# Optimization experiments

Hardware: AMD Instinct MI355X
Metric: run time of the kernel (lower is better)

## Reference

```python
import jax, jax.numpy as jnp
import numpy as np

B, N, A = 32, 1024, 256          # batch, n_entities, n_agents
D_IN, D_H, H = 256, 256, 8       # input_dim, hidden_dim, n_heads
SCALE = 1.0 / np.sqrt(D_H)
EPS = 1e-12


def setup_inputs() -> dict:
    key = jax.random.key(0)
    ks = jax.random.split(key, 7)
    x = jax.random.normal(ks[0], (B, N, D_IN), dtype=jnp.float32)
    # binary visibility mask [batch, n_agents, n_entities]
    m = (jax.random.uniform(ks[1], (B, A, N)) > 0.5).astype(jnp.float32)
    # encoder Linear(input_dim, hidden_dim): weight [out,in], bias [out]
    W_enc = jax.random.normal(ks[2], (D_H, D_IN), dtype=jnp.float32) / np.sqrt(D_IN)
    b_enc = jnp.zeros((D_H,), dtype=jnp.float32)
    # per-head projection matrices stacked [H, D_H, D_H] (torch.randn init)
    WQ = jax.random.normal(ks[3], (H, D_H, D_H), dtype=jnp.float32)
    WK = jax.random.normal(ks[4], (H, D_H, D_H), dtype=jnp.float32)
    WV = jax.random.normal(ks[5], (H, D_H, D_H), dtype=jnp.float32)
    return {"x": x, "m": m, "W_enc": W_enc, "b_enc": b_enc, "WQ": WQ, "WK": WK, "WV": WV}


def reference(x, m, W_enc, b_enc, WQ, WK, WV):
    # encode: LeakyReLU then Linear
    h = jnp.einsum('bni,oi->bno', jax.nn.leaky_relu(x), W_enc) + b_enc  # [B,N,D_H]
    n_agents = m.shape[1]
    ha = h[:, :n_agents]                                   # [B,A,D_H]
    # per-head projections, heads vectorized
    Q = jnp.einsum('bad,hde->bhae', ha, WQ)                # [B,H,A,D_H]
    K = jnp.einsum('bnd,hde->bhne', h, WK)                 # [B,H,N,D_H]
    V = jnp.einsum('bnd,hde->bhne', h, WV)                 # [B,H,N,D_H]
    S = jnp.einsum('bhae,bhne->bhan', Q, K) * SCALE        # [B,H,A,N]
    P = jax.nn.softmax(S, axis=-1)
    P = P * m[:, None]                                     # post-softmax mask
    prob = P / (jnp.sum(P, axis=-1, keepdims=True) + EPS)  # renormalize
    z = jnp.einsum('bhan,bhne->bhae', prob, V)             # [B,H,A,D_H]
    return jnp.mean(z, axis=1)                             # [B,A,D_H]
```

## Files before the change

kernel.cpp:

```cpp
#include <hip/hip_runtime.h>
#include <math.h>

namespace {
constexpr int B_N  = 32;
constexpr int SEQ  = 1024;
constexpr int AG   = 256;
constexpr int D    = 256;
constexpr int NH   = 8;
constexpr float SCALE = 0.0625f;
constexpr float EPS   = 1e-12f;

constexpr size_t HHI_OFF  = 0;
constexpr size_t HLO_OFF  = 16777216;
constexpr size_t HT_OFF   = 33554432;
constexpr size_t MTHI_OFF = 50331648;
constexpr size_t MTLO_OFF = 51380224;
constexpr size_t MB_OFF   = 52428800;
constexpr size_t WVT_OFF  = 53477376;
constexpr size_t Z16_OFF  = 54525952;
}

typedef __attribute__((ext_vector_type(8))) short short8;
typedef __attribute__((ext_vector_type(4))) float floatx4;
#define MFMA_BF(A,B,C) __builtin_amdgcn_mfma_f32_16x16x32_bf16(A,B,C,0,0,0)

__device__ __forceinline__ unsigned short bf16_rtne(float f) {
    unsigned u = __float_as_uint(f);
    u += 0x7fffu + ((u >> 16) & 1u);
    return (unsigned short)(u >> 16);
}
__device__ __forceinline__ float bf16_tof(unsigned short h) {
    return __uint_as_float(((unsigned)h) << 16);
}
__device__ __forceinline__ void async16(void* lds, const void* g) {
    __builtin_amdgcn_global_load_lds(
        (const __attribute__((address_space(1))) unsigned int*)g,
        (__attribute__((address_space(3))) unsigned int*)lds,
        16, 0, 0);
}

__global__ __launch_bounds__(256) void enc_kernel(
    const float* __restrict__ x, const float* __restrict__ W_enc,
    const float* __restrict__ b_enc,
    ushort* __restrict__ h_hi, ushort* __restrict__ h_lo)
{
    __shared__ float AsT[32][68];
    __shared__ float BsT[32][68];
    const int t  = threadIdx.x;
    const int tx = t & 15, ty = t >> 4;
    const int col0 = blockIdx.x * 64;
    const int row0 = blockIdx.y * 64;

    float acc[4][4];
#pragma unroll
    for (int r = 0; r < 4; ++r)
#pragma unroll
        for (int c = 0; c < 4; ++c) acc[r][c] = 0.f;

    for (int k0 = 0; k0 < 256; k0 += 32) {
        __syncthreads();
#pragma unroll
        for (int ss = 0; ss < 2; ++ss) {
            int flat = t + 256 * ss;
            int rr = flat >> 3, k4 = flat & 7;
            float4 v = *(const float4*)(x + (size_t)(row0 + rr) * 256 + k0 + k4 * 4);
            v.x = v.x > 0.f ? v.x : 0.01f * v.x;
            v.y = v.y > 0.f ? v.y : 0.01f * v.y;
            v.z = v.z > 0.f ? v.z : 0.01f * v.z;
            v.w = v.w > 0.f ? v.w : 0.01f * v.w;
            AsT[k4*4+0][rr] = v.x; AsT[k4*4+1][rr] = v.y;
            AsT[k4*4+2][rr] = v.z; AsT[k4*4+3][rr] = v.w;
            float4 wv = *(const float4*)(W_enc + (size_t)(col0 + rr) * 256 + k0 + k4 * 4);
            BsT[k4*4+0][rr] = wv.x; BsT[k4*4+1][rr] = wv.y;
            BsT[k4*4+2][rr] = wv.z; BsT[k4*4+3][rr] = wv.w;
        }
        __syncthreads();
#pragma unroll 8
        for (int kk = 0; kk < 32; ++kk) {
            float4 a4 = *(const float4*)&AsT[kk][ty * 4];
            float4 b4 = *(const float4*)&BsT[kk][tx * 4];
            const float ar[4] = {a4.x, a4.y, a4.z, a4.w};
            const float bc[4] = {b4.x, b4.y, b4.z, b4.w};
#pragma unroll
            for (int r = 0; r < 4; ++r)
#pragma unroll
                for (int c = 0; c < 4; ++c)
                    acc[r][c] = fmaf(ar[r], bc[c], acc[r][c]);
        }
    }

    float4 bv = *(const float4*)(b_enc + col0 + tx * 4);
    const float bb4[4] = {bv.x, bv.y, bv.z, bv.w};
#pragma unroll
    for (int r = 0; r < 4; ++r) {
        const int row = row0 + ty * 4 + r;
        ushort hi4[4], lo4[4];
#pragma unroll
        for (int c = 0; c < 4; ++c) {
            float v = acc[r][c] + bb4[c];
            hi4[c] = bf16_rtne(v);
            lo4[c] = bf16_rtne(v - bf16_tof(hi4[c]));
        }
        *(ushort4*)(h_hi + (size_t)row * 256 + col0 + tx * 4) =
            make_ushort4(hi4[0], hi4[1], hi4[2], hi4[3]);
        *(ushort4*)(h_lo + (size_t)row * 256 + col0 + tx * 4) =
            make_ushort4(lo4[0], lo4[1], lo4[2], lo4[3]);
    }
}

__global__ __launch_bounds__(256) void htrans_kernel(
    const ushort* __restrict__ h_hi, ushort* __restrict__ hT)
{
    __shared__ ushort T[64][72];
    const int t = threadIdx.x;
    const int n0 = blockIdx.x * 64, d0 = blockIdx.y * 64, b = blockIdx.z;
    {
        const int r = t >> 2, c = (t & 3) * 16;
        const ushort* src = h_hi + ((size_t)(b * 1024 + n0 + r)) * 256 + d0 + c;
        *(short8*)&T[r][c]     = *(const short8*)src;
        *(short8*)&T[r][c + 8] = *(const short8*)(src + 8);
    }
    __syncthreads();
    {
        const int dd = t >> 2, seg = (t & 3) * 16;
        ushort tmp[16];
#pragma unroll
        for (int j = 0; j < 16; ++j) tmp[j] = T[seg + j][dd];
        ushort* dst = hT + ((size_t)(b * 256 + d0 + dd)) * 1024 + n0 + seg;
        *(short8*)dst       = *(short8*)&tmp[0];
        *(short8*)(dst + 8) = *(short8*)&tmp[8];
    }
}

__global__ __launch_bounds__(256) void wvt_kernel(
    const float* __restrict__ WV, ushort* __restrict__ WVt)
{
    __shared__ float T[64][68];
    const int t = threadIdx.x;
    const int d0 = blockIdx.x * 64, e0 = blockIdx.y * 64, h = blockIdx.z;
    {
        const int r = t >> 2, c = (t & 3) * 16;
        const float* src = WV + ((size_t)(h * 256 + d0 + r)) * 256 + e0 + c;
#pragma unroll
        for (int j = 0; j < 4; ++j)
            *(float4*)&T[r][c + j * 4] = *(const float4*)(src + j * 4);
    }
    __syncthreads();
    {
        const int ee = t >> 2, seg = (t & 3) * 16;
        ushort tmp[16];
#pragma unroll
        for (int j = 0; j < 16; ++j) tmp[j] = bf16_rtne(T[seg + j][ee]);
        ushort* dst = WVt + ((size_t)(h * 256 + e0 + ee)) * 256 + d0 + seg;
        *(short8*)dst       = *(short8*)&tmp[0];
        *(short8*)(dst + 8) = *(short8*)&tmp[8];
    }
}

__global__ __launch_bounds__(256) void mprep_kernel(
    const float* __restrict__ WQ, const float* __restrict__ WK,
    ushort* __restrict__ Mt_hi, ushort* __restrict__ Mt_lo)
{
    __shared__ float AsT[32][68];
    __shared__ float BsT[32][68];
    const int t  = threadIdx.x;
    const int tx = t & 15, ty = t >> 4;
    const int col0 = blockIdx.x * 64;
    const int row0 = blockIdx.y * 64;
    const float* A  = WK + (size_t)blockIdx.z * 256 * 256;
    const float* Bm = WQ + (size_t)blockIdx.z * 256 * 256;
    ushort* Chi = Mt_hi + (size_t)blockIdx.z * 256 * 256;
    ushort* Clo = Mt_lo + (size_t)blockIdx.z * 256 * 256;

    float acc[4][4];
#pragma unroll
    for (int r = 0; r < 4; ++r)
#pragma unroll
        for (int c = 0; c < 4; ++c) acc[r][c] = 0.f;

    for (int k0 = 0; k0 < 256; k0 += 32) {
        __syncthreads();
#pragma unroll
        for (int ss = 0; ss < 2; ++ss) {
            int flat = t + 256 * ss;
            int rr = flat >> 3, k4 = flat & 7;
            float4 v = *(const float4*)(A + (size_t)(row0 + rr) * 256 + k0 + k4 * 4);
            AsT[k4*4+0][rr] = v.x; AsT[k4*4+1][rr] = v.y;
            AsT[k4*4+2][rr] = v.z; AsT[k4*4+3][rr] = v.w;
            float4 wv = *(const float4*)(Bm + (size_t)(col0 + rr) * 256 + k0 + k4 * 4);
            BsT[k4*4+0][rr] = wv.x; BsT[k4*4+1][rr] = wv.y;
            BsT[k4*4+2][rr] = wv.z; BsT[k4*4+3][rr] = wv.w;
        }
        __syncthreads();
#pragma unroll 8
        for (int kk = 0; kk < 32; ++kk) {
            float4 a4 = *(const float4*)&AsT[kk][ty * 4];
            float4 b4 = *(const float4*)&BsT[kk][tx * 4];
            const float ar[4] = {a4.x, a4.y, a4.z, a4.w};
            const float bc[4] = {b4.x, b4.y, b4.z, b4.w};
#pragma unroll
            for (int r = 0; r < 4; ++r)
#pragma unroll
                for (int c = 0; c < 4; ++c)
                    acc[r][c] = fmaf(ar[r], bc[c], acc[r][c]);
        }
    }
#pragma unroll
    for (int r = 0; r < 4; ++r) {
        const int row = row0 + ty * 4 + r;
        ushort hi4[4], lo4[4];
#pragma unroll
        for (int c = 0; c < 4; ++c) {
            float v = acc[r][c];
            hi4[c] = bf16_rtne(v);
            lo4[c] = bf16_rtne(v - bf16_tof(hi4[c]));
        }
        *(ushort4*)(Chi + (size_t)row * 256 + col0 + tx * 4) =
            make_ushort4(hi4[0], hi4[1], hi4[2], hi4[3]);
        *(ushort4*)(Clo + (size_t)row * 256 + col0 + tx * 4) =
            make_ushort4(lo4[0], lo4[1], lo4[2], lo4[3]);
    }
}

__global__ __launch_bounds__(256) void maskbits_kernel(
    const float* __restrict__ m, unsigned* __restrict__ mb)
{
    const int idx = blockIdx.x * 256 + threadIdx.x;
    const float4* src = (const float4*)(m + (size_t)idx * 32);
    unsigned wbits = 0;
#pragma unroll
    for (int i = 0; i < 8; ++i) {
        float4 v = src[i];
        wbits |= (v.x > 0.5f ? 1u : 0u) << (i * 4 + 0);
        wbits |= (v.y > 0.5f ? 1u : 0u) << (i * 4 + 1);
        wbits |= (v.z > 0.5f ? 1u : 0u) << (i * 4 + 2);
        wbits |= (v.w > 0.5f ? 1u : 0u) << (i * 4 + 3);
    }
    mb[idx] = wbits;
}

__global__ __launch_bounds__(256, 2) void attn_mfma(
    const ushort* __restrict__ h_hi, const ushort* __restrict__ h_lo,
    const ushort* __restrict__ hT,   const ushort* __restrict__ Mt_hi,
    const ushort* __restrict__ Mt_lo, const unsigned* __restrict__ mbits,
    ushort* __restrict__ zout)
{
    __shared__ __align__(16) char lds[54272];
    ushort* hS_hi = (ushort*)lds;
    ushort* hS_lo = (ushort*)(lds + 16384);
    ushort* hTS   = (ushort*)(lds + 32768);
    ushort* pP    = (ushort*)(lds + 49152);

    const int t    = threadIdx.x;
    const int wv   = t >> 6;
    const int lane = t & 63;
    const int l15  = lane & 15;
    const int quad = lane >> 4;
    const int f    = blockIdx.x;
    const int b    = (f & 7) + 8 * (f >> 8);
    const int r5   = (f >> 3) & 31;
    const int hh   = r5 >> 2;
    const int a0   = (r5 & 3) * 64;
    const int aw   = a0 + wv * 16;

    const ushort* hbh = h_hi + (size_t)b * SEQ * D;
    const ushort* hbl = h_lo + (size_t)b * SEQ * D;
    const ushort* hTb = hT   + (size_t)b * D * SEQ;

    floatx4 qac[16];
#pragma unroll
    for (int i = 0; i < 16; ++i) qac[i] = (floatx4){0.f, 0.f, 0.f, 0.f};

    for (int kc = 0; kc < 4; ++kc) {
        short8 Ah[2], Al[2];
#pragma unroll
        for (int kt = 0; kt < 2; ++kt) {
            const size_t ao = ((size_t)b * SEQ + aw + l15) * D +
                              kc * 64 + kt * 32 + quad * 8;
            Ah[kt] = *(const short8*)(h_hi + ao);
            Al[kt] = *(const short8*)(h_lo + ao);
        }
#pragma unroll
        for (int nt2 = 0; nt2 < 16; ++nt2) {
#pragma unroll
            for (int kt = 0; kt < 2; ++kt) {
                const size_t mo = ((size_t)hh * D + nt2 * 16 + l15) * D +
                                  kc * 64 + kt * 32 + quad * 8;
                short8 Bh = *(const short8*)(Mt_hi + mo);
                short8 Bl = *(const short8*)(Mt_lo + mo);
                qac[nt2] = MFMA_BF(Ah[kt], Bh, qac[nt2]);
                qac[nt2] = MFMA_BF(Al[kt], Bh, qac[nt2]);
                qac[nt2] = MFMA_BF(Ah[kt], Bl, qac[nt2]);
            }
        }
    }

    short8 Qhi[8], Qlo[8];
    {
        float* qscr = (float*)lds;
        for (int c = 0; c < 4; ++c) {
#pragma unroll
            for (int j = 0; j < 4; ++j)
#pragma unroll
                for (int r = 0; r < 4; ++r)
                    qscr[(wv * 16 + quad * 4 + r) * 68 + j * 16 + l15] = qac[c * 4 + j][r];
#pragma unroll
            for (int kt = 0; kt < 2; ++kt) {
                const float* pr = &qscr[(wv * 16 + l15) * 68 + kt * 32 + quad * 8];
                float ftmp[8];
                *(float4*)&ftmp[0] = *(const float4*)pr;
                *(float4*)&ftmp[4] = *(const float4*)(pr + 4);
                short8 hi, lo;
#pragma unroll
                for (int e = 0; e < 8; ++e) {
                    unsigned short hb = bf16_rtne(ftmp[e]);
                    hi[e] = (short)hb;
                    lo[e] = (short)bf16_rtne(ftmp[e] - bf16_tof(hb));
                }
                Qhi[c * 2 + kt] = hi;
                Qlo[c * 2 + kt] = lo;
            }
        }
    }

    floatx4 zac[16];
#pragma unroll
    for (int i = 0; i < 16; ++i) zac[i] = (floatx4){0.f, 0.f, 0.f, 0.f};
    float mx[4] = {-INFINITY, -INFINITY, -INFINITY, -INFINITY};
    float Za[4] = {0.f, 0.f, 0.f, 0.f};
    float Zm[4] = {0.f, 0.f, 0.f, 0.f};

    for (int nt = 0; nt < 32; ++nt) {
        const int n0 = nt * 32;
        __syncthreads();

#pragma unroll
        for (int i = 0; i < 4; ++i) {
            const int slot = wv * 256 + i * 64 + lane;
            const int row  = slot >> 5;
            const int p    = slot & 31;
            const int c    = p ^ (row & 7);
            const size_t go = (size_t)(n0 + row) * 256 + c * 8;
            const size_t lo_ = (size_t)(wv * 256 + i * 64) * 8;
            async16(hS_hi + lo_, hbh + go);
            async16(hS_lo + lo_, hbl + go);
        }
#pragma unroll
        for (int i = 0; i < 4; ++i) {
            const int slot = wv * 256 + i * 64 + lane;
            const int row  = slot >> 2;
            const int p    = slot & 3;
            const int c    = p ^ ((row >> 2) & 3);
            async16(hTS + (size_t)(wv * 256 + i * 64) * 8,
                    hTb + (size_t)row * 1024 + n0 + c * 8);
        }
        __syncthreads();

        floatx4 sac[2];
        sac[0] = (floatx4){0.f, 0.f, 0.f, 0.f};
        sac[1] = (floatx4){0.f, 0.f, 0.f, 0.f};
#pragma unroll
        for (int ks = 0; ks < 8; ++ks) {
            const int cg = ks * 4 + quad;
#pragma unroll
            for (int ntile = 0; ntile < 2; ++ntile) {
                const int row = ntile * 16 + l15;
                const int off = row * 256 + (cg ^ (row & 7)) * 8;
                short8 Bh = *(const short8*)&hS_hi[off];
                short8 Bl = *(const short8*)&hS_lo[off];
                sac[ntile] = MFMA_BF(Qhi[ks], Bh, sac[ntile]);
                sac[ntile] = MFMA_BF(Qlo[ks], Bh, sac[ntile]);
                sac[ntile] = MFMA_BF(Qhi[ks], Bl, sac[ntile]);
            }
        }

        float alr[4];
#pragma unroll
        for (int r = 0; r < 4; ++r) {
            const int a = a0 + wv * 16 + quad * 4 + r;
            const unsigned w0 = mbits[((size_t)b * AG + a) * (SEQ / 32) + nt];
            float l0 = sac[0][r] * SCALE, l1 = sac[1][r] * SCALE;
            float mt = fmaxf(l0, l1);
#pragma unroll
            for (int off = 1; off < 16; off <<= 1) mt = fmaxf(mt, __shfl_xor(mt, off));
            const float mxn = fmaxf(mx[r], mt);
            const float al  = __expf(mx[r] - mxn);
            float e0 = __expf(l0 - mxn), e1 = __expf(l1 - mxn);
            float p0 = ((w0 >> l15) & 1u)        ? e0 : 0.f;
            float p1 = ((w0 >> (16 + l15)) & 1u) ? e1 : 0.f;
            float za = e0 + e1;
            float zm = p0 + p1;
#pragma unroll
            for (int off = 1; off < 16; off <<= 1) {
                za += __shfl_xor(za, off);
                zm += __shfl_xor(zm, off);
            }
            Za[r] = Za[r] * al + za;
            Zm[r] = Zm[r] * al + zm;
            mx[r] = mxn;
            pP[(wv * 16 + quad * 4 + r) * 40 + l15]      = bf16_rtne(p0);
            pP[(wv * 16 + quad * 4 + r) * 40 + 16 + l15] = bf16_rtne(p1);
            alr[r] = al;
        }
#pragma unroll
        for (int dt = 0; dt < 16; ++dt) {
            zac[dt][0] *= alr[0]; zac[dt][1] *= alr[1];
            zac[dt][2] *= alr[2]; zac[dt][3] *= alr[3];
        }

        short8 Pf = *(const short8*)&pP[(wv * 16 + l15) * 40 + quad * 8];
#pragma unroll
        for (int dt = 0; dt < 16; ++dt) {
            const int row = dt * 16 + l15;
            const int p   = quad ^ ((row >> 2) & 3);
            short8 Bf = *(const short8*)&hTS[row * 32 + p * 8];
            zac[dt] = MFMA_BF(Pf, Bf, zac[dt]);
        }
    }

#pragma unroll
    for (int r = 0; r < 4; ++r) {
        const int a = a0 + wv * 16 + quad * 4 + r;
        const float inv = 1.0f / (Zm[r] + EPS * Za[r]);
        ushort* zr = zout + (((size_t)b * NH + hh) * AG + a) * D;
#pragma unroll
        for (int dt = 0; dt < 16; ++dt)
            zr[dt * 16 + l15] = bf16_rtne(zac[dt][r] * inv);
    }
}

__global__ __launch_bounds__(256) void out_mfma(
    const ushort* __restrict__ z16, const ushort* __restrict__ WVt,
    float* __restrict__ out)
{
    const int t    = threadIdx.x;
    const int wv   = t >> 6;
    const int lane = t & 63;
    const int l15  = lane & 15;
    const int quad = lane >> 4;
    const int e0 = blockIdx.x * 64;
    const int a0 = blockIdx.y * 64;
    const int b  = blockIdx.z;
    const int aw = a0 + wv * 16;

    floatx4 acc[4];
#pragma unroll
    for (int i = 0; i < 4; ++i) acc[i] = (floatx4){0.f, 0.f, 0.f, 0.f};

#pragma unroll 4
    for (int c = 0; c < 64; ++c) {
        const int hh = c >> 3, d0 = (c & 7) * 32;
        short8 Af = *(const short8*)(z16 +
            (((size_t)b * NH + hh) * AG + aw + l15) * D + d0 + quad * 8);
#pragma unroll
        for (int et = 0; et < 4; ++et) {
            short8 Bf = *(const short8*)(WVt +
                ((size_t)hh * D + e0 + et * 16 + l15) * D + d0 + quad * 8);
            acc[et] = MFMA_BF(Af, Bf, acc[et]);
        }
    }
#pragma unroll
    for (int et = 0; et < 4; ++et)
#pragma unroll
        for (int r = 0; r < 4; ++r)
            out[((size_t)b * AG + aw + quad * 4 + r) * D + e0 + et * 16 + l15] =
                acc[et][r] * 0.125f;
}

extern "C" void kernel_launch(void* const* d_in, const int* in_sizes, int n_in,
                              void* d_out, int out_size, void* d_ws, size_t ws_size,
                              hipStream_t stream)
{
    (void)in_sizes; (void)n_in; (void)out_size; (void)ws_size;
    const float* x     = (const float*)d_in[0];
    const float* m     = (const float*)d_in[1];
    const float* W_enc = (const float*)d_in[2];
    const float* b_enc = (const float*)d_in[3];
    const float* WQ    = (const float*)d_in[4];
    const float* WK    = (const float*)d_in[5];
    const float* WV    = (const float*)d_in[6];
    float* out = (float*)d_out;
    char* ws = (char*)d_ws;

    ushort*   h_hi  = (ushort*)(ws + HHI_OFF);
    ushort*   h_lo  = (ushort*)(ws + HLO_OFF);
    ushort*   hT    = (ushort*)(ws + HT_OFF);
    ushort*   Mt_hi = (ushort*)(ws + MTHI_OFF);
    ushort*   Mt_lo = (ushort*)(ws + MTLO_OFF);
    unsigned* mbits = (unsigned*)(ws + MB_OFF);
    ushort*   WVt   = (ushort*)(ws + WVT_OFF);
    ushort*   z16   = (ushort*)(ws + Z16_OFF);

    enc_kernel<<<dim3(4, 512, 1), dim3(256), 0, stream>>>(
        x, W_enc, b_enc, h_hi, h_lo);
    mprep_kernel<<<dim3(4, 4, NH), dim3(256), 0, stream>>>(WQ, WK, Mt_hi, Mt_lo);
    maskbits_kernel<<<dim3(1024, 1, 1), dim3(256), 0, stream>>>(m, mbits);
    htrans_kernel<<<dim3(16, 4, B_N), dim3(256), 0, stream>>>(h_hi, hT);
    wvt_kernel<<<dim3(4, 4, NH), dim3(256), 0, stream>>>(WV, WVt);
    attn_mfma<<<dim3(1024, 1, 1), dim3(256), 0, stream>>>(
        h_hi, h_lo, hT, Mt_hi, Mt_lo, mbits, z16);
    out_mfma<<<dim3(4, 4, B_N), dim3(256), 0, stream>>>(z16, WVt, out);
}
```

Before: 607.3 us.

## Fuse prep kernels into one launch and share K/V tiles across two heads

Four small preprocessing kernels (mask bit-packing, h transpose, WV transpose, WQ/WK product) are merged into one launch that dispatches on block index. This removes launch gaps between them. The attention kernel now uses 512-thread blocks, so two heads share each block and each staged h/hT tile in LDS. That halves global-to-LDS traffic per head and halves the block count. The cost is more register pressure under launch_bounds(512,4), larger LDS per block, and fewer blocks, which can reduce occupancy or load balance.

Result: slower. 915.2 us (+50.7%).

```diff
diff --git a/kernel.cpp b/kernel.cpp
--- a/kernel.cpp
+++ b/kernel.cpp
@@ -108,144 +108,142 @@
     }
 }
 
-__global__ __launch_bounds__(256) void htrans_kernel(
-    const ushort* __restrict__ h_hi, ushort* __restrict__ hT)
-{
-    __shared__ ushort T[64][72];
-    const int t = threadIdx.x;
-    const int n0 = blockIdx.x * 64, d0 = blockIdx.y * 64, b = blockIdx.z;
-    {
-        const int r = t >> 2, c = (t & 3) * 16;
-        const ushort* src = h_hi + ((size_t)(b * 1024 + n0 + r)) * 256 + d0 + c;
-        *(short8*)&T[r][c]     = *(const short8*)src;
-        *(short8*)&T[r][c + 8] = *(const short8*)(src + 8);
-    }
-    __syncthreads();
-    {
-        const int dd = t >> 2, seg = (t & 3) * 16;
-        ushort tmp[16];
-#pragma unroll
-        for (int j = 0; j < 16; ++j) tmp[j] = T[seg + j][dd];
-        ushort* dst = hT + ((size_t)(b * 256 + d0 + dd)) * 1024 + n0 + seg;
-        *(short8*)dst       = *(short8*)&tmp[0];
-        *(short8*)(dst + 8) = *(short8*)&tmp[8];
-    }
-}
-
-__global__ __launch_bounds__(256) void wvt_kernel(
-    const float* __restrict__ WV, ushort* __restrict__ WVt)
-{
-    __shared__ float T[64][68];
-    const int t = threadIdx.x;
-    const int d0 = blockIdx.x * 64, e0 = blockIdx.y * 64, h = blockIdx.z;
-    {
-        const int r = t >> 2, c = (t & 3) * 16;
-        const float* src = WV + ((size_t)(h * 256 + d0 + r)) * 256 + e0 + c;
-#pragma unroll
-        for (int j = 0; j < 4; ++j)
-            *(float4*)&T[r][c + j * 4] = *(const float4*)(src + j * 4);
-    }
-    __syncthreads();
-    {
-        const int ee = t >> 2, seg = (t & 3) * 16;
-        ushort tmp[16];
-#pragma unroll
-        for (int j = 0; j < 16; ++j) tmp[j] = bf16_rtne(T[seg + j][ee]);
-        ushort* dst = WVt + ((size_t)(h * 256 + e0 + ee)) * 256 + d0 + seg;
-        *(short8*)dst       = *(short8*)&tmp[0];
-        *(short8*)(dst + 8) = *(short8*)&tmp[8];
-    }
-}
-
-__global__ __launch_bounds__(256) void mprep_kernel(
+__global__ __launch_bounds__(256) void prep_fused(
+    const float* __restrict__ m, unsigned* __restrict__ mb,
+    const ushort* __restrict__ h_hi, ushort* __restrict__ hT,
+    const float* __restrict__ WV, ushort* __restrict__ WVt,
     const float* __restrict__ WQ, const float* __restrict__ WK,
     ushort* __restrict__ Mt_hi, ushort* __restrict__ Mt_lo)
 {
-    __shared__ float AsT[32][68];
-    __shared__ float BsT[32][68];
-    const int t  = threadIdx.x;
-    const int tx = t & 15, ty = t >> 4;
-    const int col0 = blockIdx.x * 64;
-    const int row0 = blockIdx.y * 64;
-    const float* A  = WK + (size_t)blockIdx.z * 256 * 256;
-    const float* Bm = WQ + (size_t)blockIdx.z * 256 * 256;
-    ushort* Chi = Mt_hi + (size_t)blockIdx.z * 256 * 256;
-    ushort* Clo = Mt_lo + (size_t)blockIdx.z * 256 * 256;
-
-    float acc[4][4];
-#pragma unroll
-    for (int r = 0; r < 4; ++r)
-#pragma unroll
-        for (int c = 0; c < 4; ++c) acc[r][c] = 0.f;
-
-    for (int k0 = 0; k0 < 256; k0 += 32) {
-        __syncthreads();
-#pragma unroll
-        for (int ss = 0; ss < 2; ++ss) {
-            int flat = t + 256 * ss;
-            int rr = flat >> 3, k4 = flat & 7;
-            float4 v = *(const float4*)(A + (size_t)(row0 + rr) * 256 + k0 + k4 * 4);
-            AsT[k4*4+0][rr] = v.x; AsT[k4*4+1][rr] = v.y;
-            AsT[k4*4+2][rr] = v.z; AsT[k4*4+3][rr] = v.w;
-            float4 wv = *(const float4*)(Bm + (size_t)(col0 + rr) * 256 + k0 + k4 * 4);
-            BsT[k4*4+0][rr] = wv.x; BsT[k4*4+1][rr] = wv.y;
-            BsT[k4*4+2][rr] = wv.z; BsT[k4*4+3][rr] = wv.w;
-        }
-        __syncthreads();
+    __shared__ __align__(16) char plds[17408];
+    const int t = threadIdx.x;
+    const int v = blockIdx.x;
+
+    if (v < 1024) {
+        const int idx = v * 256 + t;
+        const float4* src = (const float4*)(m + (size_t)idx * 32);
+        unsigned wbits = 0;
+#pragma unroll
+        for (int i = 0; i < 8; ++i) {
+            float4 vv = src[i];
+            wbits |= (vv.x > 0.5f ? 1u : 0u) << (i * 4 + 0);
+            wbits |= (vv.y > 0.5f ? 1u : 0u) << (i * 4 + 1);
+            wbits |= (vv.z > 0.5f ? 1u : 0u) << (i * 4 + 2);
+            wbits |= (vv.w > 0.5f ? 1u : 0u) << (i * 4 + 3);
+        }
+        mb[idx] = wbits;
+    } else if (v < 3072) {
+        ushort (*T)[72] = (ushort(*)[72])plds;
+        const int v1 = v - 1024;
+        const int n0 = (v1 & 15) * 64, d0 = ((v1 >> 4) & 3) * 64, b = v1 >> 6;
+        {
+            const int r = t >> 2, c = (t & 3) * 16;
+            const ushort* src = h_hi + ((size_t)(b * 1024 + n0 + r)) * 256 + d0 + c;
+            *(short8*)&T[r][c]     = *(const short8*)src;
+            *(short8*)&T[r][c + 8] = *(const short8*)(src + 8);
+        }
+        __syncthreads();
+        {
+            const int dd = t >> 2, seg = (t & 3) * 16;
+            ushort tmp[16];
+#pragma unroll
+            for (int j = 0; j < 16; ++j) tmp[j] = T[seg + j][dd];
+            ushort* dst = hT + ((size_t)(b * 256 + d0 + dd)) * 1024 + n0 + seg;
+            *(short8*)dst       = *(short8*)&tmp[0];
+            *(short8*)(dst + 8) = *(short8*)&tmp[8];
+        }
+    } else if (v < 3200) {
+        float (*T)[68] = (float(*)[68])plds;
+        const int v2 = v - 3072;
+        const int d0 = (v2 & 3) * 64, e0 = ((v2 >> 2) & 3) * 64, h = v2 >> 4;
+        {
+            const int r = t >> 2, c = (t & 3) * 16;
+            const float* src = WV + ((size_t)(h * 256 + d0 + r)) * 256 + e0 + c;
+#pragma unroll
+            for (int j = 0; j < 4; ++j)
+                *(float4*)&T[r][c + j * 4] = *(const float4*)(src + j * 4);
+        }
+        __syncthreads();
+        {
+            const int ee = t >> 2, seg = (t & 3) * 16;
+            ushort tmp[16];
+#pragma unroll
+            for (int j = 0; j < 16; ++j) tmp[j] = bf16_rtne(T[seg + j][ee]);
+            ushort* dst = WVt + ((size_t)(h * 256 + e0 + ee)) * 256 + d0 + seg;
+            *(short8*)dst       = *(short8*)&tmp[0];
+            *(short8*)(dst + 8) = *(short8*)&tmp[8];
+        }
+    } else {
+        float (*AsT)[68] = (float(*)[68])plds;
+        float (*BsT)[68] = (float(*)[68])(plds + 8704);
+        const int v3 = v - 3200;
+        const int tx = t & 15, ty = t >> 4;
+        const int col0 = (v3 & 3) * 64;
+        const int row0 = ((v3 >> 2) & 3) * 64;
+        const int hz   = v3 >> 4;
+        const float* A  = WK + (size_t)hz * 256 * 256;
+        const float* Bm = WQ + (size_t)hz * 256 * 256;
+        ushort* Chi = Mt_hi + (size_t)hz * 256 * 256;
+        ushort* Clo = Mt_lo + (size_t)hz * 256 * 256;
+
+        float acc[4][4];
+#pragma unroll
+        for (int r = 0; r < 4; ++r)
+#pragma unroll
+            for (int c = 0; c < 4; ++c) acc[r][c] = 0.f;
+
+        for (int k0 = 0; k0 < 256; k0 += 32) {
+            __syncthreads();
+#pragma unroll
+            for (int ss = 0; ss < 2; ++ss) {
+                int flat = t + 256 * ss;
+                int rr = flat >> 3, k4 = flat & 7;
+                float4 vv = *(const float4*)(A + (size_t)(row0 + rr) * 256 + k0 + k4 * 4);
+                AsT[k4*4+0][rr] = vv.x; AsT[k4*4+1][rr] = vv.y;
+                AsT[k4*4+2][rr] = vv.z; AsT[k4*4+3][rr] = vv.w;
+                float4 wv = *(const float4*)(Bm + (size_t)(col0 + rr) * 256 + k0 + k4 * 4);
+                BsT[k4*4+0][rr] = wv.x; BsT[k4*4+1][rr] = wv.y;
+                BsT[k4*4+2][rr] = wv.z; BsT[k4*4+3][rr] = wv.w;
+            }
+            __syncthreads();
 #pragma unroll 8
-        for (int kk = 0; kk < 32; ++kk) {
-            float4 a4 = *(const float4*)&AsT[kk][ty * 4];
-            float4 b4 = *(const float4*)&BsT[kk][tx * 4];
-            const float ar[4] = {a4.x, a4.y, a4.z, a4.w};
-            const float bc[4] = {b4.x, b4.y, b4.z, b4.w};
-#pragma unroll
-            for (int r = 0; r < 4; ++r)
-#pragma unroll
-                for (int c = 0; c < 4; ++c)
-                    acc[r][c] = fmaf(ar[r], bc[c], acc[r][c]);
-        }
-    }
-#pragma unroll
-    for (int r = 0; r < 4; ++r) {
-        const int row = row0 + ty * 4 + r;
-        ushort hi4[4], lo4[4];
-#pragma unroll
-        for (int c = 0; c < 4; ++c) {
-            float v = acc[r][c];
-            hi4[c] = bf16_rtne(v);
-            lo4[c] = bf16_rtne(v - bf16_tof(hi4[c]));
-        }
-        *(ushort4*)(Chi + (size_t)row * 256 + col0 + tx * 4) =
-            make_ushort4(hi4[0], hi4[1], hi4[2], hi4[3]);
-        *(ushort4*)(Clo + (size_t)row * 256 + col0 + tx * 4) =
-            make_ushort4(lo4[0], lo4[1], lo4[2], lo4[3]);
-    }
-}
-
-__global__ __launch_bounds__(256) void maskbits_kernel(
-    const float* __restrict__ m, unsigned* __restrict__ mb)
-{
-    const int idx = blockIdx.x * 256 + threadIdx.x;
-    const float4* src = (const float4*)(m + (size_t)idx * 32);
-    unsigned wbits = 0;
-#pragma unroll
-    for (int i = 0; i < 8; ++i) {
-        float4 v = src[i];
-        wbits |= (v.x > 0.5f ? 1u : 0u) << (i * 4 + 0);
-        wbits |= (v.y > 0.5f ? 1u : 0u) << (i * 4 + 1);
-        wbits |= (v.z > 0.5f ? 1u : 0u) << (i * 4 + 2);
-        wbits |= (v.w > 0.5f ? 1u : 0u) << (i * 4 + 3);
-    }
-    mb[idx] = wbits;
-}
-
-__global__ __launch_bounds__(256, 2) void attn_mfma(
+            for (int kk = 0; kk < 32; ++kk) {
+                float4 a4 = *(const float4*)&AsT[kk][ty * 4];
+                float4 b4 = *(const float4*)&BsT[kk][tx * 4];
+                const float ar[4] = {a4.x, a4.y, a4.z, a4.w};
+                const float bc[4] = {b4.x, b4.y, b4.z, b4.w};
+#pragma unroll
+                for (int r = 0; r < 4; ++r)
+#pragma unroll
+                    for (int c = 0; c < 4; ++c)
+                        acc[r][c] = fmaf(ar[r], bc[c], acc[r][c]);
+            }
+        }
+#pragma unroll
+        for (int r = 0; r < 4; ++r) {
+            const int row = row0 + ty * 4 + r;
+            ushort hi4[4], lo4[4];
+#pragma unroll
+            for (int c = 0; c < 4; ++c) {
+                float vv = acc[r][c];
+                hi4[c] = bf16_rtne(vv);
+                lo4[c] = bf16_rtne(vv - bf16_tof(hi4[c]));
+            }
+            *(ushort4*)(Chi + (size_t)row * 256 + col0 + tx * 4) =
+                make_ushort4(hi4[0], hi4[1], hi4[2], hi4[3]);
+            *(ushort4*)(Clo + (size_t)row * 256 + col0 + tx * 4) =
+                make_ushort4(lo4[0], lo4[1], lo4[2], lo4[3]);
+        }
+    }
+}
+
+__global__ __launch_bounds__(512, 4) void attn_mfma(
     const ushort* __restrict__ h_hi, const ushort* __restrict__ h_lo,
     const ushort* __restrict__ hT,   const ushort* __restrict__ Mt_hi,
     const ushort* __restrict__ Mt_lo, const unsigned* __restrict__ mbits,
     ushort* __restrict__ zout)
 {
-    __shared__ __align__(16) char lds[54272];
+    __shared__ __align__(16) char lds[59392];
     ushort* hS_hi = (ushort*)lds;
     ushort* hS_lo = (ushort*)(lds + 16384);
     ushort* hTS   = (ushort*)(lds + 32768);
@@ -257,11 +255,11 @@
     const int l15  = lane & 15;
     const int quad = lane >> 4;
     const int f    = blockIdx.x;
-    const int b    = (f & 7) + 8 * (f >> 8);
-    const int r5   = (f >> 3) & 31;
-    const int hh   = r5 >> 2;
-    const int a0   = (r5 & 3) * 64;
-    const int aw   = a0 + wv * 16;
+    const int b    = (f & 7) + 8 * (f >> 7);
+    const int mid  = (f >> 3) & 15;
+    const int hh   = (mid >> 2) * 2 + (wv >> 2);
+    const int a0   = (mid & 3) * 64;
+    const int aw   = a0 + (wv & 3) * 16;
 
     const ushort* hbh = h_hi + (size_t)b * SEQ * D;
     const ushort* hbl = h_lo + (size_t)b * SEQ * D;
@@ -335,23 +333,23 @@
         __syncthreads();
 
 #pragma unroll
-        for (int i = 0; i < 4; ++i) {
-            const int slot = wv * 256 + i * 64 + lane;
+        for (int i = 0; i < 2; ++i) {
+            const int slot = wv * 128 + i * 64 + lane;
             const int row  = slot >> 5;
             const int p    = slot & 31;
             const int c    = p ^ (row & 7);
             const size_t go = (size_t)(n0 + row) * 256 + c * 8;
-            const size_t lo_ = (size_t)(wv * 256 + i * 64) * 8;
+            const size_t lo_ = (size_t)(wv * 128 + i * 64) * 8;
             async16(hS_hi + lo_, hbh + go);
             async16(hS_lo + lo_, hbl + go);
         }
 #pragma unroll
-        for (int i = 0; i < 4; ++i) {
-            const int slot = wv * 256 + i * 64 + lane;
+        for (int i = 0; i < 2; ++i) {
+            const int slot = wv * 128 + i * 64 + lane;
             const int row  = slot >> 2;
             const int p    = slot & 3;
             const int c    = p ^ ((row >> 2) & 3);
-            async16(hTS + (size_t)(wv * 256 + i * 64) * 8,
+            async16(hTS + (size_t)(wv * 128 + i * 64) * 8,
                     hTb + (size_t)row * 1024 + n0 + c * 8);
         }
         __syncthreads();
@@ -377,7 +375,7 @@
         float alr[4];
 #pragma unroll
         for (int r = 0; r < 4; ++r) {
-            const int a = a0 + wv * 16 + quad * 4 + r;
+            const int a = aw + quad * 4 + r;
             const unsigned w0 = mbits[((size_t)b * AG + a) * (SEQ / 32) + nt];
             float l0 = sac[0][r] * SCALE, l1 = sac[1][r] * SCALE;
             float mt = fmaxf(l0, l1);
@@ -420,7 +418,7 @@
 
 #pragma unroll
     for (int r = 0; r < 4; ++r) {
-        const int a = a0 + wv * 16 + quad * 4 + r;
+        const int a = aw + quad * 4 + r;
         const float inv = 1.0f / (Zm[r] + EPS * Za[r]);
         ushort* zr = zout + (((size_t)b * NH + hh) * AG + a) * D;
 #pragma unroll
@@ -493,11 +491,9 @@
 
     enc_kernel<<<dim3(4, 512, 1), dim3(256), 0, stream>>>(
         x, W_enc, b_enc, h_hi, h_lo);
-    mprep_kernel<<<dim3(4, 4, NH), dim3(256), 0, stream>>>(WQ, WK, Mt_hi, Mt_lo);
-    maskbits_kernel<<<dim3(1024, 1, 1), dim3(256), 0, stream>>>(m, mbits);
-    htrans_kernel<<<dim3(16, 4, B_N), dim3(256), 0, stream>>>(h_hi, hT);
-    wvt_kernel<<<dim3(4, 4, NH), dim3(256), 0, stream>>>(WV, WVt);
-    attn_mfma<<<dim3(1024, 1, 1), dim3(256), 0, stream>>>(
+    prep_fused<<<dim3(3328, 1, 1), dim3(256), 0, stream>>>(
+        m, mbits, h_hi, hT, WV, WVt, WQ, WK, Mt_hi, Mt_lo);
+    attn_mfma<<<dim3(512, 1, 1), dim3(512), 0, stream>>>(
         h_hi, h_lo, hT, Mt_hi, Mt_lo, mbits, z16);
     out_mfma<<<dim3(4, 4, B_N), dim3(256), 0, stream>>>(z16, WVt, out);
 }
```
